# Optimization experiments

Measured on AMD Instinct MI355X. Metric: run time of the kernel, lower is better.

The kernel has to match this reference:

```python
import jax, jax.numpy as jnp
import numpy as np

B, D, L = 2048, 4096, 3
# Fixed 5-node star graph hardcoded in the source module
SRC = jnp.array([1, 2, 3, 4])
DST = jnp.array([0, 0, 0, 0])


def setup_inputs() -> dict:
    key = jax.random.key(0)
    ks = jax.random.split(key, 13)
    inp = {}
    names = ["pair_now", "person_1_now", "person_2_now", "scene_now",
             "pair_pre", "person_1_pre", "person_2_pre", "scene_pre"]
    for i, n in enumerate(names):
        inp[n] = jax.random.normal(ks[i], (B, D), dtype=jnp.float32)
    # GatedGraphConv per-layer message weight [L, D, D]
    inp["W"] = jax.random.normal(ks[8], (L, D, D), dtype=jnp.float32) * 0.02
    # GRUCell parameters (torch layout: [3D, D] for ih and hh, biases [3D])
    inp["w_ih"] = jax.random.normal(ks[9], (3 * D, D), dtype=jnp.float32) * 0.02
    inp["w_hh"] = jax.random.normal(ks[10], (3 * D, D), dtype=jnp.float32) * 0.02
    inp["b_ih"] = jax.random.normal(ks[11], (3 * D,), dtype=jnp.float32) * 0.02
    inp["b_hh"] = jax.random.normal(ks[12], (3 * D,), dtype=jnp.float32) * 0.02
    return inp


def _forward(pair_now, person_1_now, person_2_now, scene_now,
             pair_pre, person_1_pre, person_2_pre, scene_pre,
             W, w_ih, w_hh, b_ih, b_hh):
    # mean over batch dim -> one D-vector per stream
    pre_means = jnp.stack([pair_pre.mean(0), person_1_pre.mean(0),
                           person_2_pre.mean(0), scene_pre.mean(0)])  # [4, D]
    now_means = jnp.stack([pair_now.mean(0), person_1_now.mean(0),
                           person_2_now.mean(0), scene_now.mean(0)])  # [4, D]

    def ggc(node0):
        # node features: [node0, pair_pre, p1_pre, p2_pre, scene_pre] -> [5, D]
        h = jnp.concatenate([node0[None], pre_means], axis=0)

        def step(h, Wl):
            msg = h @ Wl                                   # [5, D]
            agg = jnp.zeros_like(h).at[DST].add(msg[SRC])  # star: sum into node 0
            # torch GRUCell
            gi = agg @ w_ih.T + b_ih                       # [5, 3D]
            gh = h @ w_hh.T + b_hh
            i_r, i_z, i_n = jnp.split(gi, 3, axis=-1)
            h_r, h_z, h_n = jnp.split(gh, 3, axis=-1)
            r = jax.nn.sigmoid(i_r + h_r)
            z = jax.nn.sigmoid(i_z + h_z)
            n = jnp.tanh(i_n + r * h_n)
            return (1.0 - z) * n + z * h, None

        h, _ = jax.lax.scan(step, h, W)
        return h[0]  # node-0 output [D]

    outs = jax.vmap(ggc)(now_means)                 # [4, D]
    losses = jnp.mean((outs - pre_means) ** 2, -1)  # MSE per stream
    return jnp.sum(losses) * 10.0


def reference(pair_now, person_1_now, person_2_now, scene_now,
              pair_pre, person_1_pre, person_2_pre, scene_pre,
              W, w_ih, w_hh, b_ih, b_hh):
    return _forward(pair_now, person_1_now, person_2_now, scene_now,
                    pair_pre, person_1_pre, person_2_pre, scene_pre,
                    W, w_ih, w_hh, b_ih, b_hh)
```

## Files before the change

### kernel.cpp

```cpp
#include <hip/hip_runtime.h>
#include <hip/hip_bf16.h>

#define B  2048
#define D  4096
#define D3 12288
#define L  3

struct Ptrs8 { const float* p[8]; };

typedef float        f32x4 __attribute__((ext_vector_type(4)));
typedef unsigned int u32x2 __attribute__((ext_vector_type(2)));
typedef unsigned short u16x4 __attribute__((ext_vector_type(4)));

__device__ __forceinline__ f32x4 ldnt4(const float* p) {
    return __builtin_nontemporal_load(reinterpret_cast<const f32x4*>(p));
}
__device__ __forceinline__ f32x4 ld4(const float* p) {
    return *reinterpret_cast<const f32x4*>(p);
}

__device__ __forceinline__ unsigned short f2bf(float f) {
    union { float f; unsigned int u; } v; v.f = f;
    unsigned int r = v.u + 0x7FFFu + ((v.u >> 16) & 1u);
    return (unsigned short)(r >> 16);
}
__device__ __forceinline__ float bf_lo(unsigned int u) {
    union { unsigned int u; float f; } v; v.u = u << 16; return v.f;
}
__device__ __forceinline__ float bf_hi(unsigned int u) {
    union { unsigned int u; float f; } v; v.u = u & 0xFFFF0000u; return v.f;
}

__global__ void k_mean_partial(Ptrs8 in, float* __restrict__ partials) {
    const int cc = blockIdx.x, rc = blockIdx.y, m = blockIdx.z;
    const float* __restrict__ src = in.p[m];
    const int col0 = cc * 1024 + threadIdx.x * 4;
    const int row0 = rc * 128;
    f32x4 acc = {0.f, 0.f, 0.f, 0.f};
    for (int r = 0; r < 128; ++r) {
        const f32x4 v = ldnt4(src + (size_t)(row0 + r) * D + col0);
        acc += v;
    }
    *reinterpret_cast<f32x4*>(partials + ((size_t)(m * 16 + rc)) * D + col0) = acc;
}

__global__ void k_mean_finalize(const float* __restrict__ partials,
                                float* __restrict__ means,
                                float* __restrict__ h,
                                float* __restrict__ svec) {
    const int d = blockIdx.x * 256 + threadIdx.x;
    float mv[8];
    #pragma unroll
    for (int m = 0; m < 8; ++m) {
        float s = 0.f;
        #pragma unroll
        for (int rc = 0; rc < 16; ++rc) s += partials[(size_t)(m * 16 + rc) * D + d];
        mv[m] = s * (1.0f / (float)B);
        means[m * D + d] = mv[m];
    }
    float ssum = 0.f;
    #pragma unroll
    for (int j = 0; j < 4; ++j) {
        h[j * D + d] = mv[4 + j];
        ssum += mv[4 + j];
    }
    #pragma unroll
    for (int s = 0; s < 4; ++s)
        h[(4 + s) * D + d] = mv[s];
    svec[d] = ssum;
}

__global__ void k_aggmsg_partial(const float* __restrict__ Wl,
                                 const float* __restrict__ svec,
                                 float* __restrict__ partials) {
    const int col0 = blockIdx.x * 1024 + threadIdx.x * 4;
    const int row0 = blockIdx.y * 64;
    f32x4 acc = {0.f, 0.f, 0.f, 0.f};
    for (int r = 0; r < 64; ++r) {
        const float sv = svec[row0 + r];
        const f32x4 w = ldnt4(Wl + (size_t)(row0 + r) * D + col0);
        acc += sv * w;
    }
    *reinterpret_cast<f32x4*>(partials + (size_t)blockIdx.y * D + col0) = acc;
}

__global__ void k_aggmsg_reduce(const float* __restrict__ partials,
                                float* __restrict__ aggmsg) {
    const int d = blockIdx.x * 256 + threadIdx.x;
    float s = 0.f;
    #pragma unroll
    for (int r = 0; r < 64; ++r) s += partials[(size_t)r * D + d];
    aggmsg[d] = s;
}

__global__ __launch_bounds__(256, 4)
void k_gates_f32(const float* __restrict__ w_ih,
                 const float* __restrict__ w_hh,
                 const float* __restrict__ h,
                 const float* __restrict__ aggmsg,
                 const float* __restrict__ b_ih,
                 const float* __restrict__ b_hh,
                 float* __restrict__ gi0,
                 float* __restrict__ gh,
                 unsigned short* __restrict__ wih_bf,
                 unsigned short* __restrict__ whh_bf) {
    const int gwid = (blockIdx.x * blockDim.x + threadIdx.x) >> 6;
    const int lane = threadIdx.x & 63;
    if (gwid < 3072) {
        const int k0 = gwid * 4;
        float acc[4][8] = {};
        for (int i = 0; i < 16; ++i) {
            const int idx = i * 256 + lane * 4;
            f32x4 w[4];
            #pragma unroll
            for (int r = 0; r < 4; ++r)
                w[r] = ldnt4(w_hh + (size_t)(k0 + r) * D + idx);
            #pragma unroll
            for (int r = 0; r < 4; ++r) {
                u16x4 wb;
                wb.x = f2bf(w[r].x); wb.y = f2bf(w[r].y);
                wb.z = f2bf(w[r].z); wb.w = f2bf(w[r].w);
                *reinterpret_cast<u16x4*>(whh_bf + (size_t)(k0 + r) * D + idx) = wb;
            }
            f32x4 hv[8];
            #pragma unroll
            for (int j = 0; j < 8; ++j) hv[j] = ld4(h + j * D + idx);
            #pragma unroll
            for (int r = 0; r < 4; ++r)
                #pragma unroll
                for (int j = 0; j < 8; ++j)
                    acc[r][j] += w[r].x * hv[j].x + w[r].y * hv[j].y
                               + w[r].z * hv[j].z + w[r].w * hv[j].w;
        }
        #pragma unroll
        for (int r = 0; r < 4; ++r)
            #pragma unroll
            for (int j = 0; j < 8; ++j) {
                float v = acc[r][j];
                #pragma unroll
                for (int off = 32; off; off >>= 1) v += __shfl_xor(v, off);
                if (lane == 0) gh[(size_t)j * D3 + k0 + r] = v + b_hh[k0 + r];
            }
    } else {
        const int k0 = (gwid - 3072) * 4;
        float acc[4] = {0.f, 0.f, 0.f, 0.f};
        for (int i = 0; i < 16; ++i) {
            const int idx = i * 256 + lane * 4;
            const f32x4 a = ld4(aggmsg + idx);
            #pragma unroll
            for (int r = 0; r < 4; ++r) {
                const f32x4 w = ldnt4(w_ih + (size_t)(k0 + r) * D + idx);
                u16x4 wb;
                wb.x = f2bf(w.x); wb.y = f2bf(w.y);
                wb.z = f2bf(w.z); wb.w = f2bf(w.w);
                *reinterpret_cast<u16x4*>(wih_bf + (size_t)(k0 + r) * D + idx) = wb;
                acc[r] += w.x * a.x + w.y * a.y + w.z * a.z + w.w * a.w;
            }
        }
        #pragma unroll
        for (int r = 0; r < 4; ++r) {
            float v = acc[r];
            #pragma unroll
            for (int off = 32; off; off >>= 1) v += __shfl_xor(v, off);
            if (lane == 0) gi0[k0 + r] = v + b_ih[k0 + r];
        }
    }
}

__global__ __launch_bounds__(256, 4)
void k_gates_bf(const unsigned short* __restrict__ wih_bf,
                const unsigned short* __restrict__ whh_bf,
                const float* __restrict__ h,
                const float* __restrict__ aggmsg,
                const float* __restrict__ b_ih,
                const float* __restrict__ b_hh,
                float* __restrict__ gi0,
                float* __restrict__ gh) {
    const int gwid = (blockIdx.x * blockDim.x + threadIdx.x) >> 6;
    const int lane = threadIdx.x & 63;
    if (gwid < 3072) {
        const int k0 = gwid * 4;
        float acc[4][8] = {};
        for (int i = 0; i < 16; ++i) {
            const int idx = i * 256 + lane * 4;
            u32x2 wu[4];
            #pragma unroll
            for (int r = 0; r < 4; ++r)
                wu[r] = *reinterpret_cast<const u32x2*>(
                    whh_bf + (size_t)(k0 + r) * D + idx);
            f32x4 hv[8];
            #pragma unroll
            for (int j = 0; j < 8; ++j) hv[j] = ld4(h + j * D + idx);
            #pragma unroll
            for (int r = 0; r < 4; ++r) {
                const float w0 = bf_lo(wu[r].x), w1 = bf_hi(wu[r].x);
                const float w2 = bf_lo(wu[r].y), w3 = bf_hi(wu[r].y);
                #pragma unroll
                for (int j = 0; j < 8; ++j)
                    acc[r][j] += w0 * hv[j].x + w1 * hv[j].y
                               + w2 * hv[j].z + w3 * hv[j].w;
            }
        }
        #pragma unroll
        for (int r = 0; r < 4; ++r)
            #pragma unroll
            for (int j = 0; j < 8; ++j) {
                float v = acc[r][j];
                #pragma unroll
                for (int off = 32; off; off >>= 1) v += __shfl_xor(v, off);
                if (lane == 0) gh[(size_t)j * D3 + k0 + r] = v + b_hh[k0 + r];
            }
    } else {
        const int k0 = (gwid - 3072) * 4;
        float acc[4] = {0.f, 0.f, 0.f, 0.f};
        for (int i = 0; i < 16; ++i) {
            const int idx = i * 256 + lane * 4;
            const f32x4 a = ld4(aggmsg + idx);
            #pragma unroll
            for (int r = 0; r < 4; ++r) {
                const u32x2 wu = *reinterpret_cast<const u32x2*>(
                    wih_bf + (size_t)(k0 + r) * D + idx);
                acc[r] += bf_lo(wu.x) * a.x + bf_hi(wu.x) * a.y
                        + bf_lo(wu.y) * a.z + bf_hi(wu.y) * a.w;
            }
        }
        #pragma unroll
        for (int r = 0; r < 4; ++r) {
            float v = acc[r];
            #pragma unroll
            for (int off = 32; off; off >>= 1) v += __shfl_xor(v, off);
            if (lane == 0) gi0[k0 + r] = v + b_ih[k0 + r];
        }
    }
}

__device__ __forceinline__ float sigmoidf_(float x) {
    return 1.0f / (1.0f + __expf(-x));
}

__global__ void k_gru(const float* __restrict__ gi0,
                      const float* __restrict__ gh,
                      const float* __restrict__ b_ih,
                      float* __restrict__ h,
                      float* __restrict__ svec) {
    const int d = blockIdx.x * 256 + threadIdx.x;
    const float bir = b_ih[d], biz = b_ih[D + d], bin = b_ih[2 * D + d];
    const float gir = gi0[d],  giz = gi0[D + d],  gin = gi0[2 * D + d];
    float ssum = 0.f;
    #pragma unroll
    for (int j = 0; j < 8; ++j) {
        const float ir = (j < 4) ? bir : gir;
        const float iz = (j < 4) ? biz : giz;
        const float in = (j < 4) ? bin : gin;
        const float hr = gh[(size_t)j * D3 + d];
        const float hz = gh[(size_t)j * D3 + D + d];
        const float hn = gh[(size_t)j * D3 + 2 * D + d];
        const float hv = h[j * D + d];
        const float r = sigmoidf_(ir + hr);
        const float z = sigmoidf_(iz + hz);
        const float n = tanhf(in + r * hn);
        const float hnew = (1.f - z) * n + z * hv;
        h[j * D + d] = hnew;
        if (j < 4) ssum += hnew;
    }
    svec[d] = ssum;
}

__global__ void k_loss(const float* __restrict__ h,
                       const float* __restrict__ means,
                       float* __restrict__ out) {
    __shared__ float red[4];
    float acc = 0.f;
    for (int idx = threadIdx.x; idx < 4 * D; idx += 256) {
        const int s = idx >> 12;
        const int d = idx & (D - 1);
        const float diff = h[(4 + s) * D + d] - means[(4 + s) * D + d];
        acc += diff * diff;
    }
    #pragma unroll
    for (int off = 32; off; off >>= 1) acc += __shfl_xor(acc, off);
    const int wave = threadIdx.x >> 6, lane = threadIdx.x & 63;
    if (lane == 0) red[wave] = acc;
    __syncthreads();
    if (threadIdx.x == 0)
        out[0] = (red[0] + red[1] + red[2] + red[3]) * (10.0f / (float)D);
}

extern "C" void kernel_launch(void* const* d_in, const int* in_sizes, int n_in,
                              void* d_out, int out_size, void* d_ws, size_t ws_size,
                              hipStream_t stream) {
    const float* W    = (const float*)d_in[8];
    const float* w_ih = (const float*)d_in[9];
    const float* w_hh = (const float*)d_in[10];
    const float* b_ih = (const float*)d_in[11];
    const float* b_hh = (const float*)d_in[12];

    float* ws     = (float*)d_ws;
    float* mpart  = ws;
    float* means  = mpart  + 8 * 16 * D;
    float* h      = means  + 8 * D;
    float* svec   = h      + 8 * D;
    float* apart  = svec   + D;
    float* aggmsg = apart  + 64 * D;
    float* gi0    = aggmsg + D;
    float* gh     = gi0    + D3;
    float* wbase  = gh     + 8 * D3;
    unsigned short* wih_bf = (unsigned short*)wbase;
    unsigned short* whh_bf = wih_bf + (size_t)D3 * D;

    Ptrs8 in8;
    for (int i = 0; i < 8; ++i) in8.p[i] = (const float*)d_in[i];

    k_mean_partial<<<dim3(4, 16, 8), 256, 0, stream>>>(in8, mpart);
    k_mean_finalize<<<16, 256, 0, stream>>>(mpart, means, h, svec);

    for (int l = 0; l < L; ++l) {
        const float* Wl = W + (size_t)l * D * D;
        k_aggmsg_partial<<<dim3(4, 64), 256, 0, stream>>>(Wl, svec, apart);
        k_aggmsg_reduce<<<16, 256, 0, stream>>>(apart, aggmsg);
        if (l == 0)
            k_gates_f32<<<1536, 256, 0, stream>>>(w_ih, w_hh, h, aggmsg,
                                                  b_ih, b_hh, gi0, gh,
                                                  wih_bf, whh_bf);
        else
            k_gates_bf<<<1536, 256, 0, stream>>>(wih_bf, whh_bf, h, aggmsg,
                                                 b_ih, b_hh, gi0, gh);
        k_gru<<<16, 256, 0, stream>>>(gi0, gh, b_ih, h, svec);
    }

    k_loss<<<1, 256, 0, stream>>>(h, means, (float*)d_out);
}
```

Before: 390.3 us.

## Stage GRU gate weights through LDS with async double buffering and widen reductions

The gate GEMV kernels now load 16-row weight tiles into shared memory with global_load_lds, double-buffered so the next tile streams in while the current one is used. Each block handles only w_hh or only w_ih, and launch_bounds no longer forces four blocks per CU. The mean and aggmsg partial kernels use more row chunks with four independent accumulators, which adds memory-level parallelism but doubles or quadruples the partial buffers that the single-pass reduce kernels must read. This trades larger reduction passes and added __syncthreads for better bandwidth on the dominant weight streams.

```diff
diff --git a/kernel.cpp b/kernel.cpp
--- a/kernel.cpp
+++ b/kernel.cpp
@@ -5,11 +5,12 @@
 #define D  4096
 #define D3 12288
 #define L  3
+#define BK 256
 
 struct Ptrs8 { const float* p[8]; };
 
-typedef float        f32x4 __attribute__((ext_vector_type(4)));
-typedef unsigned int u32x2 __attribute__((ext_vector_type(2)));
+typedef float          f32x4 __attribute__((ext_vector_type(4)));
+typedef unsigned int   u32x2 __attribute__((ext_vector_type(2)));
 typedef unsigned short u16x4 __attribute__((ext_vector_type(4)));
 
 __device__ __forceinline__ f32x4 ldnt4(const float* p) {
@@ -17,6 +18,11 @@
 }
 __device__ __forceinline__ f32x4 ld4(const float* p) {
     return *reinterpret_cast<const f32x4*>(p);
+}
+__device__ __forceinline__ void gload16(const void* g, void* l) {
+    __builtin_amdgcn_global_load_lds(
+        (const __attribute__((address_space(1))) unsigned int*)g,
+        (__attribute__((address_space(3))) unsigned int*)l, 16, 0, 0);
 }
 
 __device__ __forceinline__ unsigned short f2bf(float f) {
@@ -35,13 +41,17 @@
     const int cc = blockIdx.x, rc = blockIdx.y, m = blockIdx.z;
     const float* __restrict__ src = in.p[m];
     const int col0 = cc * 1024 + threadIdx.x * 4;
-    const int row0 = rc * 128;
-    f32x4 acc = {0.f, 0.f, 0.f, 0.f};
-    for (int r = 0; r < 128; ++r) {
-        const f32x4 v = ldnt4(src + (size_t)(row0 + r) * D + col0);
-        acc += v;
-    }
-    *reinterpret_cast<f32x4*>(partials + ((size_t)(m * 16 + rc)) * D + col0) = acc;
+    const size_t base = (size_t)(rc * 32) * D + col0;
+    f32x4 a0 = {0,0,0,0}, a1 = {0,0,0,0}, a2 = {0,0,0,0}, a3 = {0,0,0,0};
+    #pragma unroll
+    for (int r = 0; r < 32; r += 4) {
+        a0 += ldnt4(src + base + (size_t)(r + 0) * D);
+        a1 += ldnt4(src + base + (size_t)(r + 1) * D);
+        a2 += ldnt4(src + base + (size_t)(r + 2) * D);
+        a3 += ldnt4(src + base + (size_t)(r + 3) * D);
+    }
+    const f32x4 acc = (a0 + a1) + (a2 + a3);
+    *reinterpret_cast<f32x4*>(partials + ((size_t)(m * 64 + rc)) * D + col0) = acc;
 }
 
 __global__ void k_mean_finalize(const float* __restrict__ partials,
@@ -53,8 +63,7 @@
     #pragma unroll
     for (int m = 0; m < 8; ++m) {
         float s = 0.f;
-        #pragma unroll
-        for (int rc = 0; rc < 16; ++rc) s += partials[(size_t)(m * 16 + rc) * D + d];
+        for (int rc = 0; rc < 64; ++rc) s += partials[(size_t)(m * 64 + rc) * D + d];
         mv[m] = s * (1.0f / (float)B);
         means[m * D + d] = mv[m];
     }
@@ -74,13 +83,16 @@
                                  const float* __restrict__ svec,
                                  float* __restrict__ partials) {
     const int col0 = blockIdx.x * 1024 + threadIdx.x * 4;
-    const int row0 = blockIdx.y * 64;
-    f32x4 acc = {0.f, 0.f, 0.f, 0.f};
-    for (int r = 0; r < 64; ++r) {
-        const float sv = svec[row0 + r];
-        const f32x4 w = ldnt4(Wl + (size_t)(row0 + r) * D + col0);
-        acc += sv * w;
-    }
+    const int row0 = blockIdx.y * 16;
+    f32x4 a0 = {0,0,0,0}, a1 = {0,0,0,0}, a2 = {0,0,0,0}, a3 = {0,0,0,0};
+    #pragma unroll
+    for (int r = 0; r < 16; r += 4) {
+        a0 += svec[row0 + r + 0] * ldnt4(Wl + (size_t)(row0 + r + 0) * D + col0);
+        a1 += svec[row0 + r + 1] * ldnt4(Wl + (size_t)(row0 + r + 1) * D + col0);
+        a2 += svec[row0 + r + 2] * ldnt4(Wl + (size_t)(row0 + r + 2) * D + col0);
+        a3 += svec[row0 + r + 3] * ldnt4(Wl + (size_t)(row0 + r + 3) * D + col0);
+    }
+    const f32x4 acc = (a0 + a1) + (a2 + a3);
     *reinterpret_cast<f32x4*>(partials + (size_t)blockIdx.y * D + col0) = acc;
 }
 
@@ -88,12 +100,11 @@
                                 float* __restrict__ aggmsg) {
     const int d = blockIdx.x * 256 + threadIdx.x;
     float s = 0.f;
-    #pragma unroll
-    for (int r = 0; r < 64; ++r) s += partials[(size_t)r * D + d];
+    for (int r = 0; r < 256; ++r) s += partials[(size_t)r * D + d];
     aggmsg[d] = s;
 }
 
-__global__ __launch_bounds__(256, 4)
+__global__ __launch_bounds__(256)
 void k_gates_f32(const float* __restrict__ w_ih,
                  const float* __restrict__ w_hh,
                  const float* __restrict__ h,
@@ -104,70 +115,82 @@
                  float* __restrict__ gh,
                  unsigned short* __restrict__ wih_bf,
                  unsigned short* __restrict__ whh_bf) {
-    const int gwid = (blockIdx.x * blockDim.x + threadIdx.x) >> 6;
-    const int lane = threadIdx.x & 63;
-    if (gwid < 3072) {
-        const int k0 = gwid * 4;
-        float acc[4][8] = {};
-        for (int i = 0; i < 16; ++i) {
-            const int idx = i * 256 + lane * 4;
-            f32x4 w[4];
-            #pragma unroll
-            for (int r = 0; r < 4; ++r)
-                w[r] = ldnt4(w_hh + (size_t)(k0 + r) * D + idx);
-            #pragma unroll
-            for (int r = 0; r < 4; ++r) {
-                u16x4 wb;
-                wb.x = f2bf(w[r].x); wb.y = f2bf(w[r].y);
-                wb.z = f2bf(w[r].z); wb.w = f2bf(w[r].w);
-                *reinterpret_cast<u16x4*>(whh_bf + (size_t)(k0 + r) * D + idx) = wb;
+    __shared__ float sw[2][16][BK];
+    const bool is_ih = (blockIdx.x >= 768);
+    const int  kbase = (is_ih ? blockIdx.x - 768 : blockIdx.x) * 16;
+    const float* __restrict__ wsrc = is_ih ? w_ih : w_hh;
+    unsigned short* __restrict__ wdst = is_ih ? wih_bf : whh_bf;
+    const int wid = threadIdx.x >> 6, lane = threadIdx.x & 63;
+
+    auto stage = [&](int t, int b) {
+        #pragma unroll
+        for (int rr = 0; rr < 4; ++rr) {
+            const int row = wid * 4 + rr;
+            gload16(wsrc + (size_t)(kbase + row) * D + t * BK + lane * 4,
+                    &sw[b][row][0]);
+        }
+    };
+
+    float acc[4][8] = {};
+    stage(0, 0);
+    __syncthreads();
+    for (int t = 0; t < 16; ++t) {
+        if (t + 1 < 16) stage(t + 1, (t + 1) & 1);
+        const int cb = t & 1;
+        f32x4 wreg[4];
+        #pragma unroll
+        for (int rr = 0; rr < 4; ++rr) {
+            const int row = wid * 4 + rr;
+            wreg[rr] = *reinterpret_cast<const f32x4*>(&sw[cb][row][lane * 4]);
+            u16x4 wb;
+            wb.x = f2bf(wreg[rr].x); wb.y = f2bf(wreg[rr].y);
+            wb.z = f2bf(wreg[rr].z); wb.w = f2bf(wreg[rr].w);
+            *reinterpret_cast<u16x4*>(
+                wdst + (size_t)(kbase + row) * D + t * BK + lane * 4) = wb;
+        }
+        if (!is_ih) {
+            #pragma unroll
+            for (int j = 0; j < 8; ++j) {
+                const f32x4 hv = ld4(h + j * D + t * BK + lane * 4);
+                #pragma unroll
+                for (int rr = 0; rr < 4; ++rr)
+                    acc[rr][j] += wreg[rr].x * hv.x + wreg[rr].y * hv.y
+                                + wreg[rr].z * hv.z + wreg[rr].w * hv.w;
             }
-            f32x4 hv[8];
-            #pragma unroll
-            for (int j = 0; j < 8; ++j) hv[j] = ld4(h + j * D + idx);
-            #pragma unroll
-            for (int r = 0; r < 4; ++r)
-                #pragma unroll
-                for (int j = 0; j < 8; ++j)
-                    acc[r][j] += w[r].x * hv[j].x + w[r].y * hv[j].y
-                               + w[r].z * hv[j].z + w[r].w * hv[j].w;
-        }
-        #pragma unroll
-        for (int r = 0; r < 4; ++r)
+        } else {
+            const f32x4 av = ld4(aggmsg + t * BK + lane * 4);
+            #pragma unroll
+            for (int rr = 0; rr < 4; ++rr)
+                acc[rr][0] += wreg[rr].x * av.x + wreg[rr].y * av.y
+                            + wreg[rr].z * av.z + wreg[rr].w * av.w;
+        }
+        __syncthreads();
+    }
+
+    if (!is_ih) {
+        #pragma unroll
+        for (int rr = 0; rr < 4; ++rr)
             #pragma unroll
             for (int j = 0; j < 8; ++j) {
-                float v = acc[r][j];
+                float v = acc[rr][j];
                 #pragma unroll
                 for (int off = 32; off; off >>= 1) v += __shfl_xor(v, off);
-                if (lane == 0) gh[(size_t)j * D3 + k0 + r] = v + b_hh[k0 + r];
+                if (lane == 0)
+                    gh[(size_t)j * D3 + kbase + wid * 4 + rr] = v + b_hh[kbase + wid * 4 + rr];
             }
     } else {
-        const int k0 = (gwid - 3072) * 4;
-        float acc[4] = {0.f, 0.f, 0.f, 0.f};
-        for (int i = 0; i < 16; ++i) {
-            const int idx = i * 256 + lane * 4;
-            const f32x4 a = ld4(aggmsg + idx);
-            #pragma unroll
-            for (int r = 0; r < 4; ++r) {
-                const f32x4 w = ldnt4(w_ih + (size_t)(k0 + r) * D + idx);
-                u16x4 wb;
-                wb.x = f2bf(w.x); wb.y = f2bf(w.y);
-                wb.z = f2bf(w.z); wb.w = f2bf(w.w);
-                *reinterpret_cast<u16x4*>(wih_bf + (size_t)(k0 + r) * D + idx) = wb;
-                acc[r] += w.x * a.x + w.y * a.y + w.z * a.z + w.w * a.w;
-            }
-        }
-        #pragma unroll
-        for (int r = 0; r < 4; ++r) {
-            float v = acc[r];
+        #pragma unroll
+        for (int rr = 0; rr < 4; ++rr) {
+            float v = acc[rr][0];
             #pragma unroll
             for (int off = 32; off; off >>= 1) v += __shfl_xor(v, off);
-            if (lane == 0) gi0[k0 + r] = v + b_ih[k0 + r];
-        }
-    }
-}
-
-__global__ __launch_bounds__(256, 4)
+            if (lane == 0)
+                gi0[kbase + wid * 4 + rr] = v + b_ih[kbase + wid * 4 + rr];
+        }
+    }
+}
+
+__global__ __launch_bounds__(256)
 void k_gates_bf(const unsigned short* __restrict__ wih_bf,
                 const unsigned short* __restrict__ whh_bf,
                 const float* __restrict__ h,
@@ -176,60 +199,74 @@
                 const float* __restrict__ b_hh,
                 float* __restrict__ gi0,
                 float* __restrict__ gh) {
-    const int gwid = (blockIdx.x * blockDim.x + threadIdx.x) >> 6;
-    const int lane = threadIdx.x & 63;
-    if (gwid < 3072) {
-        const int k0 = gwid * 4;
-        float acc[4][8] = {};
-        for (int i = 0; i < 16; ++i) {
-            const int idx = i * 256 + lane * 4;
-            u32x2 wu[4];
-            #pragma unroll
-            for (int r = 0; r < 4; ++r)
-                wu[r] = *reinterpret_cast<const u32x2*>(
-                    whh_bf + (size_t)(k0 + r) * D + idx);
-            f32x4 hv[8];
-            #pragma unroll
-            for (int j = 0; j < 8; ++j) hv[j] = ld4(h + j * D + idx);
-            #pragma unroll
-            for (int r = 0; r < 4; ++r) {
-                const float w0 = bf_lo(wu[r].x), w1 = bf_hi(wu[r].x);
-                const float w2 = bf_lo(wu[r].y), w3 = bf_hi(wu[r].y);
+    __shared__ unsigned short sw[2][16][BK];
+    const bool is_ih = (blockIdx.x >= 768);
+    const int  kbase = (is_ih ? blockIdx.x - 768 : blockIdx.x) * 16;
+    const unsigned short* __restrict__ wsrc = is_ih ? wih_bf : whh_bf;
+    const int wid = threadIdx.x >> 6, lane = threadIdx.x & 63;
+
+    auto stage = [&](int t, int b) {
+        #pragma unroll
+        for (int c = 0; c < 2; ++c) {
+            const int row = wid * 4 + c * 2;
+            gload16(wsrc + (size_t)(kbase + row + (lane >> 5)) * D
+                         + t * BK + (lane & 31) * 8,
+                    &sw[b][row][0]);
+        }
+    };
+
+    float acc[4][8] = {};
+    stage(0, 0);
+    __syncthreads();
+    for (int t = 0; t < 16; ++t) {
+        if (t + 1 < 16) stage(t + 1, (t + 1) & 1);
+        const int cb = t & 1;
+        float wf[4][4];
+        #pragma unroll
+        for (int rr = 0; rr < 4; ++rr) {
+            const u32x2 wu = *reinterpret_cast<const u32x2*>(
+                &sw[cb][wid * 4 + rr][lane * 4]);
+            wf[rr][0] = bf_lo(wu.x); wf[rr][1] = bf_hi(wu.x);
+            wf[rr][2] = bf_lo(wu.y); wf[rr][3] = bf_hi(wu.y);
+        }
+        if (!is_ih) {
+            #pragma unroll
+            for (int j = 0; j < 8; ++j) {
+                const f32x4 hv = ld4(h + j * D + t * BK + lane * 4);
                 #pragma unroll
-                for (int j = 0; j < 8; ++j)
-                    acc[r][j] += w0 * hv[j].x + w1 * hv[j].y
-                               + w2 * hv[j].z + w3 * hv[j].w;
+                for (int rr = 0; rr < 4; ++rr)
+                    acc[rr][j] += wf[rr][0] * hv.x + wf[rr][1] * hv.y
+                                + wf[rr][2] * hv.z + wf[rr][3] * hv.w;
             }
-        }
-        #pragma unroll
-        for (int r = 0; r < 4; ++r)
+        } else {
+            const f32x4 av = ld4(aggmsg + t * BK + lane * 4);
+            #pragma unroll
+            for (int rr = 0; rr < 4; ++rr)
+                acc[rr][0] += wf[rr][0] * av.x + wf[rr][1] * av.y
+                            + wf[rr][2] * av.z + wf[rr][3] * av.w;
+        }
+        __syncthreads();
+    }
+
+    if (!is_ih) {
+        #pragma unroll
+        for (int rr = 0; rr < 4; ++rr)
             #pragma unroll
             for (int j = 0; j < 8; ++j) {
-                float v = acc[r][j];
+                float v = acc[rr][j];
                 #pragma unroll
                 for (int off = 32; off; off >>= 1) v += __shfl_xor(v, off);
-                if (lane == 0) gh[(size_t)j * D3 + k0 + r] = v + b_hh[k0 + r];
+                if (lane == 0)
+                    gh[(size_t)j * D3 + kbase + wid * 4 + rr] = v + b_hh[kbase + wid * 4 + rr];
             }
     } else {
-        const int k0 = (gwid - 3072) * 4;
-        float acc[4] = {0.f, 0.f, 0.f, 0.f};
-        for (int i = 0; i < 16; ++i) {
-            const int idx = i * 256 + lane * 4;
-            const f32x4 a = ld4(aggmsg + idx);
-            #pragma unroll
-            for (int r = 0; r < 4; ++r) {
-                const u32x2 wu = *reinterpret_cast<const u32x2*>(
-                    wih_bf + (size_t)(k0 + r) * D + idx);
-                acc[r] += bf_lo(wu.x) * a.x + bf_hi(wu.x) * a.y
-                        + bf_lo(wu.y) * a.z + bf_hi(wu.y) * a.w;
-            }
-        }
-        #pragma unroll
-        for (int r = 0; r < 4; ++r) {
-            float v = acc[r];
+        #pragma unroll
+        for (int rr = 0; rr < 4; ++rr) {
+            float v = acc[rr][0];
             #pragma unroll
             for (int off = 32; off; off >>= 1) v += __shfl_xor(v, off);
-            if (lane == 0) gi0[k0 + r] = v + b_ih[k0 + r];
+            if (lane == 0)
+                gi0[kbase + wid * 4 + rr] = v + b_ih[kbase + wid * 4 + rr];
         }
     }
 }
@@ -297,11 +334,11 @@
 
     float* ws     = (float*)d_ws;
     float* mpart  = ws;
-    float* means  = mpart  + 8 * 16 * D;
+    float* means  = mpart  + 8 * 64 * D;
     float* h      = means  + 8 * D;
     float* svec   = h      + 8 * D;
     float* apart  = svec   + D;
-    float* aggmsg = apart  + 64 * D;
+    float* aggmsg = apart  + 256 * D;
     float* gi0    = aggmsg + D;
     float* gh     = gi0    + D3;
     float* wbase  = gh     + 8 * D3;
@@ -311,12 +348,12 @@
     Ptrs8 in8;
     for (int i = 0; i < 8; ++i) in8.p[i] = (const float*)d_in[i];
 
-    k_mean_partial<<<dim3(4, 16, 8), 256, 0, stream>>>(in8, mpart);
+    k_mean_partial<<<dim3(4, 64, 8), 256, 0, stream>>>(in8, mpart);
     k_mean_finalize<<<16, 256, 0, stream>>>(mpart, means, h, svec);
 
     for (int l = 0; l < L; ++l) {
         const float* Wl = W + (size_t)l * D * D;
-        k_aggmsg_partial<<<dim3(4, 64), 256, 0, stream>>>(Wl, svec, apart);
+        k_aggmsg_partial<<<dim3(4, 256), 256, 0, stream>>>(Wl, svec, apart);
         k_aggmsg_reduce<<<16, 256, 0, stream>>>(apart, aggmsg);
         if (l == 0)
             k_gates_f32<<<1536, 256, 0, stream>>>(w_ih, w_hh, h, aggmsg,
```

After: 397.5 us. Within noise of the previous version (+1.9%).
